# Optimization experiments

Hardware: AMD Instinct MI355X
Metric: run time of the kernel (lower is better)

Reference implementation:

```python
import jax, jax.numpy as jnp
import numpy as np

B, S, D, H = 4, 2048, 1024, 16
DH = D // H  # 64


def setup_inputs() -> dict:
    key = jax.random.key(0)
    ks = jax.random.split(key, 8)
    sc = 1.0 / np.sqrt(D)
    return {
        "hidden_states": jax.random.normal(ks[0], (B, S, D), jnp.float32),
        "attention_mask": jnp.zeros((B, 1, 1, S), jnp.float32),
        "Wq": jax.random.normal(ks[1], (D, D), jnp.float32) * sc,
        "bq": jnp.zeros((D,), jnp.float32),
        "Wk": jax.random.normal(ks[2], (D, D), jnp.float32) * sc,
        "bk": jnp.zeros((D,), jnp.float32),
        "Wv": jax.random.normal(ks[3], (D, D), jnp.float32) * sc,
        "bv": jnp.zeros((D,), jnp.float32),
    }


def _heads(x):
    # [B,S,D] -> [B,H,S,DH]
    b, s, _ = x.shape
    return x.reshape(b, s, H, DH).transpose(0, 2, 1, 3)


def reference(hidden_states, attention_mask, Wq, bq, Wk, bk, Wv, bv):
    q = _heads(hidden_states @ Wq + bq)
    k = _heads(hidden_states @ Wk + bk)
    v = _heads(hidden_states @ Wv + bv)
    scores = jnp.einsum('bhqd,bhkd->bhqk', q, k) / jnp.sqrt(jnp.float32(DH))
    scores = scores + attention_mask  # additive mask, broadcast
    probs = jax.nn.softmax(scores, axis=-1)  # dropout is identity in eval
    out = jnp.einsum('bhqk,bhkd->bhqd', probs, v)
    b, h, s, dh = out.shape
    return out.transpose(0, 2, 1, 3).reshape(b, s, h * dh)
```

## Files before the change

### kernel.cpp

```cpp
#include <hip/hip_runtime.h>
#include <hip/hip_bf16.h>
#include <cstdint>

typedef _Float16 f16;
typedef f16 f16x8 __attribute__((ext_vector_type(8)));
typedef f16 f16x4 __attribute__((ext_vector_type(4)));
typedef float f32x4 __attribute__((ext_vector_type(4)));

#define MFMA16(a, b, c) __builtin_amdgcn_mfma_f32_16x16x32_f16((a), (b), (c), 0, 0, 0)

constexpr int Bc = 4, Sc = 2048, Dc = 1024, Hc = 16, DHc = 64;

typedef __attribute__((address_space(1))) const uint32_t gbl_u32;
typedef __attribute__((address_space(3))) uint32_t lds_u32;
__device__ __forceinline__ void gld_lds16(const void* g, void* l) {
  __builtin_amdgcn_global_load_lds((gbl_u32*)g, (lds_u32*)l, 16, 0, 0);
}

__global__ __launch_bounds__(256) void cast_w_kernel(
    const float* __restrict__ Wq, const float* __restrict__ Wk,
    const float* __restrict__ Wv, f16* __restrict__ Wt) {
  __shared__ __align__(16) f16 T[64][66];
  const int z = blockIdx.z;
  const float* W = (z == 0) ? Wq : (z == 1) ? Wk : Wv;
  const int n0 = blockIdx.x * 64, k0 = blockIdx.y * 64;
  const int t = threadIdx.x;
#pragma unroll
  for (int p = 0; p < 4; p++) {
    int idx = t + p * 256;
    int r = idx >> 4, c = idx & 15;
    float4 v = *(const float4*)(W + (size_t)(k0 + r) * Dc + n0 + c * 4);
    T[r][c * 4 + 0] = (f16)v.x;
    T[r][c * 4 + 1] = (f16)v.y;
    T[r][c * 4 + 2] = (f16)v.z;
    T[r][c * 4 + 3] = (f16)v.w;
  }
  __syncthreads();
#pragma unroll
  for (int p = 0; p < 2; p++) {
    int idx = t + p * 256;
    int n = idx >> 3, c = idx & 7;
    f16x8 tmp;
#pragma unroll
    for (int j = 0; j < 8; j++) tmp[j] = T[c * 8 + j][n];
    *(f16x8*)(Wt + ((size_t)z * Dc + n0 + n) * Dc + k0 + c * 8) = tmp;
  }
}

__global__ __launch_bounds__(256) void cast_x_kernel(const float* __restrict__ X,
                                                     f16* __restrict__ X16) {
  size_t i = ((size_t)blockIdx.x * 256 + threadIdx.x) * 8;
  float4 a = *(const float4*)(X + i);
  float4 b = *(const float4*)(X + i + 4);
  f16x8 h;
  h[0] = (f16)a.x; h[1] = (f16)a.y; h[2] = (f16)a.z; h[3] = (f16)a.w;
  h[4] = (f16)b.x; h[5] = (f16)b.y; h[6] = (f16)b.z; h[7] = (f16)b.w;
  *(f16x8*)(X16 + i) = h;
}

__global__ __launch_bounds__(256) void qkv_gemm_kernel(
    const f16* __restrict__ X16, const f16* __restrict__ Wt,
    const float* __restrict__ bq, const float* __restrict__ bk,
    const float* __restrict__ bv, f16* __restrict__ Qo, f16* __restrict__ Ko,
    f16* __restrict__ Vo) {
  const int z = blockIdx.z;
  const f16* W = Wt + (size_t)z * Dc * Dc;
  const float* bias = (z == 0) ? bq : (z == 1) ? bk : bv;

  const int n0 = blockIdx.x * 128, m0 = blockIdx.y * 128;
  __shared__ __align__(16) f16 Xs[128 * 32];
  __shared__ __align__(16) f16 Ws[128 * 32];

  const int t = threadIdx.x;
  const int wave = t >> 6, lane = t & 63;
  const int l16 = lane & 15, quad = lane >> 4;
  const int wm = (wave >> 1) * 64, wn = (wave & 1) * 64;

  f32x4 acc[4][4];
#pragma unroll
  for (int i = 0; i < 4; i++)
#pragma unroll
    for (int j = 0; j < 4; j++) acc[i][j] = (f32x4){0.f, 0.f, 0.f, 0.f};

  for (int k0 = 0; k0 < Dc; k0 += 32) {
#pragma unroll
    for (int p = 0; p < 2; p++) {
      int cb = p * 256 + wave * 64;
      int chunk = cb + lane;
      int row = chunk >> 2, c8 = (chunk & 3) * 8;
      gld_lds16(X16 + (size_t)(m0 + row) * Dc + k0 + c8, (f16*)Xs + (size_t)cb * 8);
      gld_lds16(W + (size_t)(n0 + row) * Dc + k0 + c8, (f16*)Ws + (size_t)cb * 8);
    }
    __syncthreads();

    f16x8 aF[4], bF[4];
#pragma unroll
    for (int mt = 0; mt < 4; mt++)
      aF[mt] = *(const f16x8*)(&Xs[(wm + mt * 16 + l16) * 32 + quad * 8]);
#pragma unroll
    for (int nt = 0; nt < 4; nt++)
      bF[nt] = *(const f16x8*)(&Ws[(wn + nt * 16 + l16) * 32 + quad * 8]);
#pragma unroll
    for (int mt = 0; mt < 4; mt++)
#pragma unroll
      for (int nt = 0; nt < 4; nt++)
        acc[mt][nt] = MFMA16(aF[mt], bF[nt], acc[mt][nt]);
    __syncthreads();
  }

#pragma unroll
  for (int nt = 0; nt < 4; nt++) {
    int col = n0 + wn + nt * 16 + l16;
    float bval = bias[col];
    int h = col >> 6, d = col & 63;
    if (z == 2) {
#pragma unroll
      for (int mt = 0; mt < 4; mt++) {
        int m = m0 + wm + mt * 16 + quad * 4;
        int b = m >> 11, sbase = m & 2047;
        f16x4 pk;
#pragma unroll
        for (int r = 0; r < 4; r++) pk[r] = (f16)(acc[mt][nt][r] + bval);
        *(f16x4*)(Vo + (((size_t)(b * Hc + h)) * DHc + d) * Sc + sbase) = pk;
      }
    } else {
      const float sc = (z == 0) ? 0.125f : 1.0f;
      f16* O = (z == 0) ? Qo : Ko;
#pragma unroll
      for (int mt = 0; mt < 4; mt++) {
#pragma unroll
        for (int r = 0; r < 4; r++) {
          int m = m0 + wm + mt * 16 + quad * 4 + r;
          int b = m >> 11, s = m & 2047;
          O[(((size_t)(b * Hc + h)) * Sc + s) * DHc + d] =
              (f16)((acc[mt][nt][r] + bval) * sc);
        }
      }
    }
  }
}

__global__ __launch_bounds__(256) void flash_kernel(
    const f16* __restrict__ Q, const f16* __restrict__ K,
    const f16* __restrict__ Vt, const float* __restrict__ mask,
    float* __restrict__ out) {
  const int bh = blockIdx.y;
  const int b = bh >> 4, h = bh & 15;
  const int t = threadIdx.x;
  const int wave = t >> 6, lane = t & 63;
  const int l16 = lane & 15, quad = lane >> 4;
  const int qbase = blockIdx.x * 128 + wave * 32;

  __shared__ __align__(16) f16 Ks[2][4096];
  __shared__ __align__(16) f16 Vs[2][4096];
  __shared__ __align__(16) float Ms[2048];
  __shared__ __align__(16) f16 Pbuf[4][16][76];

  const f16* Kb = K + (size_t)bh * Sc * DHc;
  const f16* Vb = Vt + (size_t)bh * DHc * Sc;
  const float* mrow = mask + (size_t)b * Sc;

  const int qsw8 = (quad ^ ((l16 >> 1) & 3)) * 8;

  auto stageKV = [&](int c0, int buf) {
#pragma unroll
    for (int p = 0; p < 2; p++) {
      int cb = p * 256 + wave * 64;
      int i = cb + lane;
      int half = i >> 8, row = (i >> 2) & 63, q8 = i & 3;
      int q8g = q8 ^ ((row >> 1) & 3);
      gld_lds16(Kb + (size_t)(c0 + row) * DHc + half * 32 + q8g * 8,
                &Ks[buf][cb * 8]);
      gld_lds16(Vb + (size_t)row * Sc + c0 + half * 32 + q8g * 8,
                &Vs[buf][cb * 8]);
    }
  };

  f16x8 qa[2][2];
#pragma unroll
  for (int mt = 0; mt < 2; mt++) {
    const f16* qb = Q + ((size_t)bh * Sc + qbase + mt * 16 + l16) * DHc;
    qa[mt][0] = *(const f16x8*)(qb + quad * 8);
    qa[mt][1] = *(const f16x8*)(qb + 32 + quad * 8);
  }

  stageKV(0, 0);
#pragma unroll
  for (int p = 0; p < 2; p++) {
    int cb = p * 256 + wave * 64;
    gld_lds16(mrow + (size_t)(cb + lane) * 4, &Ms[cb * 4]);
  }
  __syncthreads();

  float l_acc[2] = {0.f, 0.f};
  f32x4 o[2][4];
#pragma unroll
  for (int mt = 0; mt < 2; mt++)
#pragma unroll
    for (int dt = 0; dt < 4; dt++) o[mt][dt] = (f32x4){0.f, 0.f, 0.f, 0.f};

  for (int c = 0; c < 32; c++) {
    const int buf = c & 1;
    if (c < 31) stageKV((c + 1) * 64, buf ^ 1);

    f16x8 ka[4][2];
#pragma unroll
    for (int nt = 0; nt < 4; nt++) {
      int rb = (nt * 16 + l16) * 32 + qsw8;
      ka[nt][0] = *(const f16x8*)(&Ks[buf][rb]);
      ka[nt][1] = *(const f16x8*)(&Ks[buf][2048 + rb]);
    }
    float4 mv[4];
#pragma unroll
    for (int nt = 0; nt < 4; nt++)
      mv[nt] = *(const float4*)(&Ms[c * 64 + nt * 16 + quad * 4]);

    f32x4 s0[4];
#pragma unroll
    for (int nt = 0; nt < 4; nt++) {
      f32x4 a = (f32x4){mv[nt].x, mv[nt].y, mv[nt].z, mv[nt].w};
      a = MFMA16(ka[nt][0], qa[0][0], a);
      a = MFMA16(ka[nt][1], qa[0][1], a);
      s0[nt] = a;
    }
    {
      float ls = 0.f;
#pragma unroll
      for (int nt = 0; nt < 4; nt++) {
        f16x4 pk;
#pragma unroll
        for (int r = 0; r < 4; r++) {
          float p = __expf(s0[nt][r]);
          ls += p;
          pk[r] = (f16)p;
        }
        *(f16x4*)(&Pbuf[wave][l16][nt * 16 + quad * 4]) = pk;
      }
      l_acc[0] += ls;
    }

    f32x4 s1[4];
#pragma unroll
    for (int nt = 0; nt < 4; nt++) {
      f32x4 a = (f32x4){mv[nt].x, mv[nt].y, mv[nt].z, mv[nt].w};
      a = MFMA16(ka[nt][0], qa[1][0], a);
      a = MFMA16(ka[nt][1], qa[1][1], a);
      s1[nt] = a;
    }

    f16x8 pa0, pa1;
    {
      const f16* prow = &Pbuf[wave][l16][0];
      f16x4 a0 = *(const f16x4*)(prow + quad * 8);
      f16x4 a1 = *(const f16x4*)(prow + quad * 8 + 4);
      f16x4 b0 = *(const f16x4*)(prow + 32 + quad * 8);
      f16x4 b1 = *(const f16x4*)(prow + 32 + quad * 8 + 4);
      pa0 = __builtin_shufflevector(a0, a1, 0, 1, 2, 3, 4, 5, 6, 7);
      pa1 = __builtin_shufflevector(b0, b1, 0, 1, 2, 3, 4, 5, 6, 7);
    }
    f16x8 vb[4][2];
#pragma unroll
    for (int dt = 0; dt < 4; dt++) {
      int rb = (dt * 16 + l16) * 32 + qsw8;
      vb[dt][0] = *(const f16x8*)(&Vs[buf][rb]);
      vb[dt][1] = *(const f16x8*)(&Vs[buf][2048 + rb]);
    }
#pragma unroll
    for (int dt = 0; dt < 4; dt++) {
      o[0][dt] = MFMA16(pa0, vb[dt][0], o[0][dt]);
      o[0][dt] = MFMA16(pa1, vb[dt][1], o[0][dt]);
    }

    {
      float ls = 0.f;
#pragma unroll
      for (int nt = 0; nt < 4; nt++) {
        f16x4 pk;
#pragma unroll
        for (int r = 0; r < 4; r++) {
          float p = __expf(s1[nt][r]);
          ls += p;
          pk[r] = (f16)p;
        }
        *(f16x4*)(&Pbuf[wave][l16][nt * 16 + quad * 4]) = pk;
      }
      l_acc[1] += ls;
    }
    {
      const f16* prow = &Pbuf[wave][l16][0];
      f16x4 a0 = *(const f16x4*)(prow + quad * 8);
      f16x4 a1 = *(const f16x4*)(prow + quad * 8 + 4);
      f16x4 b0 = *(const f16x4*)(prow + 32 + quad * 8);
      f16x4 b1 = *(const f16x4*)(prow + 32 + quad * 8 + 4);
      f16x8 qa0p = __builtin_shufflevector(a0, a1, 0, 1, 2, 3, 4, 5, 6, 7);
      f16x8 qa1p = __builtin_shufflevector(b0, b1, 0, 1, 2, 3, 4, 5, 6, 7);
#pragma unroll
      for (int dt = 0; dt < 4; dt++) {
        o[1][dt] = MFMA16(qa0p, vb[dt][0], o[1][dt]);
        o[1][dt] = MFMA16(qa1p, vb[dt][1], o[1][dt]);
      }
    }

    __syncthreads();
  }

#pragma unroll
  for (int mt = 0; mt < 2; mt++) {
    l_acc[mt] += __shfl_xor(l_acc[mt], 16);
    l_acc[mt] += __shfl_xor(l_acc[mt], 32);
  }
#pragma unroll
  for (int mt = 0; mt < 2; mt++) {
    float inv[4];
#pragma unroll
    for (int r = 0; r < 4; r++)
      inv[r] = 1.0f / __shfl(l_acc[mt], quad * 4 + r);
#pragma unroll
    for (int dt = 0; dt < 4; dt++) {
      int col = h * 64 + dt * 16 + l16;
#pragma unroll
      for (int r = 0; r < 4; r++) {
        int row = qbase + mt * 16 + quad * 4 + r;
        out[((size_t)b * Sc + row) * Dc + col] = o[mt][dt][r] * inv[r];
      }
    }
  }
}

extern "C" void kernel_launch(void* const* d_in, const int* in_sizes, int n_in,
                              void* d_out, int out_size, void* d_ws,
                              size_t ws_size, hipStream_t stream) {
  (void)in_sizes; (void)n_in; (void)out_size; (void)ws_size;
  const float* hidden = (const float*)d_in[0];
  const float* mask   = (const float*)d_in[1];
  const float* Wq     = (const float*)d_in[2];
  const float* bq     = (const float*)d_in[3];
  const float* Wk     = (const float*)d_in[4];
  const float* bk     = (const float*)d_in[5];
  const float* Wv     = (const float*)d_in[6];
  const float* bv     = (const float*)d_in[7];
  float* out = (float*)d_out;

  uint8_t* w = (uint8_t*)d_ws;
  f16* Wt   = (f16*)(w);
  f16* X16  = (f16*)(w + (size_t)6 * 1024 * 1024);
  f16* Q16  = (f16*)(w + (size_t)22 * 1024 * 1024);
  f16* K16  = (f16*)(w + (size_t)38 * 1024 * 1024);
  f16* Vt16 = (f16*)(w + (size_t)54 * 1024 * 1024);

  cast_w_kernel<<<dim3(16, 16, 3), 256, 0, stream>>>(Wq, Wk, Wv, Wt);
  cast_x_kernel<<<4096, 256, 0, stream>>>(hidden, X16);
  qkv_gemm_kernel<<<dim3(8, 64, 3), 256, 0, stream>>>(X16, Wt, bq, bk, bv,
                                                      Q16, K16, Vt16);
  flash_kernel<<<dim3(16, 64), 256, 0, stream>>>(Q16, K16, Vt16, mask, out);
}
```

Baseline: 287.2 us.

## Keep P in registers via 16x16x16 MFMA, drop LDS P round-trip and mask staging

```diff
diff --git a/kernel.cpp b/kernel.cpp
--- a/kernel.cpp
+++ b/kernel.cpp
@@ -8,6 +8,7 @@
 typedef float f32x4 __attribute__((ext_vector_type(4)));
 
 #define MFMA16(a, b, c) __builtin_amdgcn_mfma_f32_16x16x32_f16((a), (b), (c), 0, 0, 0)
+#define MFMA16K16(a, b, c) __builtin_amdgcn_mfma_f32_16x16x16f16((a), (b), (c), 0, 0, 0)
 
 constexpr int Bc = 4, Sc = 2048, Dc = 1024, Hc = 16, DHc = 64;
 
@@ -153,14 +154,13 @@
 
   __shared__ __align__(16) f16 Ks[2][4096];
   __shared__ __align__(16) f16 Vs[2][4096];
-  __shared__ __align__(16) float Ms[2048];
-  __shared__ __align__(16) f16 Pbuf[4][16][76];
 
   const f16* Kb = K + (size_t)bh * Sc * DHc;
   const f16* Vb = Vt + (size_t)bh * DHc * Sc;
   const float* mrow = mask + (size_t)b * Sc;
 
   const int qsw8 = (quad ^ ((l16 >> 1) & 3)) * 8;
+  const int vsw = (l16 >> 1) & 3;
 
   auto stageKV = [&](int c0, int buf) {
 #pragma unroll
@@ -185,11 +185,6 @@
   }
 
   stageKV(0, 0);
-#pragma unroll
-  for (int p = 0; p < 2; p++) {
-    int cb = p * 256 + wave * 64;
-    gld_lds16(mrow + (size_t)(cb + lane) * 4, &Ms[cb * 4]);
-  }
   __syncthreads();
 
   float l_acc[2] = {0.f, 0.f};
@@ -201,6 +196,10 @@
 
   for (int c = 0; c < 32; c++) {
     const int buf = c & 1;
+    float4 mv[4];
+#pragma unroll
+    for (int nt = 0; nt < 4; nt++)
+      mv[nt] = *(const float4*)(mrow + c * 64 + nt * 16 + quad * 4);
     if (c < 31) stageKV((c + 1) * 64, buf ^ 1);
 
     f16x8 ka[4][2];
@@ -210,94 +209,46 @@
       ka[nt][0] = *(const f16x8*)(&Ks[buf][rb]);
       ka[nt][1] = *(const f16x8*)(&Ks[buf][2048 + rb]);
     }
-    float4 mv[4];
-#pragma unroll
-    for (int nt = 0; nt < 4; nt++)
-      mv[nt] = *(const float4*)(&Ms[c * 64 + nt * 16 + quad * 4]);
-
-    f32x4 s0[4];
+
+    f32x4 s0[4], s1[4];
 #pragma unroll
     for (int nt = 0; nt < 4; nt++) {
       f32x4 a = (f32x4){mv[nt].x, mv[nt].y, mv[nt].z, mv[nt].w};
       a = MFMA16(ka[nt][0], qa[0][0], a);
       a = MFMA16(ka[nt][1], qa[0][1], a);
       s0[nt] = a;
-    }
-    {
-      float ls = 0.f;
+      f32x4 a2 = (f32x4){mv[nt].x, mv[nt].y, mv[nt].z, mv[nt].w};
+      a2 = MFMA16(ka[nt][0], qa[1][0], a2);
+      a2 = MFMA16(ka[nt][1], qa[1][1], a2);
+      s1[nt] = a2;
+    }
+
+    f16x4 pA[2][4];
+#pragma unroll
+    for (int nt = 0; nt < 4; nt++) {
+      float ls0 = 0.f, ls1 = 0.f;
+      f16x4 p0, p1;
+#pragma unroll
+      for (int r = 0; r < 4; r++) {
+        float e0 = __expf(s0[nt][r]);
+        float e1 = __expf(s1[nt][r]);
+        ls0 += e0; ls1 += e1;
+        p0[r] = (f16)e0; p1[r] = (f16)e1;
+      }
+      pA[0][nt] = p0; pA[1][nt] = p1;
+      l_acc[0] += ls0; l_acc[1] += ls1;
+    }
+
+#pragma unroll
+    for (int dt = 0; dt < 4; dt++) {
+      int dh = dt * 16 + l16;
 #pragma unroll
       for (int nt = 0; nt < 4; nt++) {
-        f16x4 pk;
-#pragma unroll
-        for (int r = 0; r < 4; r++) {
-          float p = __expf(s0[nt][r]);
-          ls += p;
-          pk[r] = (f16)p;
-        }
-        *(f16x4*)(&Pbuf[wave][l16][nt * 16 + quad * 4]) = pk;
-      }
-      l_acc[0] += ls;
-    }
-
-    f32x4 s1[4];
-#pragma unroll
-    for (int nt = 0; nt < 4; nt++) {
-      f32x4 a = (f32x4){mv[nt].x, mv[nt].y, mv[nt].z, mv[nt].w};
-      a = MFMA16(ka[nt][0], qa[1][0], a);
-      a = MFMA16(ka[nt][1], qa[1][1], a);
-      s1[nt] = a;
-    }
-
-    f16x8 pa0, pa1;
-    {
-      const f16* prow = &Pbuf[wave][l16][0];
-      f16x4 a0 = *(const f16x4*)(prow + quad * 8);
-      f16x4 a1 = *(const f16x4*)(prow + quad * 8 + 4);
-      f16x4 b0 = *(const f16x4*)(prow + 32 + quad * 8);
-      f16x4 b1 = *(const f16x4*)(prow + 32 + quad * 8 + 4);
-      pa0 = __builtin_shufflevector(a0, a1, 0, 1, 2, 3, 4, 5, 6, 7);
-      pa1 = __builtin_shufflevector(b0, b1, 0, 1, 2, 3, 4, 5, 6, 7);
-    }
-    f16x8 vb[4][2];
-#pragma unroll
-    for (int dt = 0; dt < 4; dt++) {
-      int rb = (dt * 16 + l16) * 32 + qsw8;
-      vb[dt][0] = *(const f16x8*)(&Vs[buf][rb]);
-      vb[dt][1] = *(const f16x8*)(&Vs[buf][2048 + rb]);
-    }
-#pragma unroll
-    for (int dt = 0; dt < 4; dt++) {
-      o[0][dt] = MFMA16(pa0, vb[dt][0], o[0][dt]);
-      o[0][dt] = MFMA16(pa1, vb[dt][1], o[0][dt]);
-    }
-
-    {
-      float ls = 0.f;
-#pragma unroll
-      for (int nt = 0; nt < 4; nt++) {
-        f16x4 pk;
-#pragma unroll
-        for (int r = 0; r < 4; r++) {
-          float p = __expf(s1[nt][r]);
-          ls += p;
-          pk[r] = (f16)p;
-        }
-        *(f16x4*)(&Pbuf[wave][l16][nt * 16 + quad * 4]) = pk;
-      }
-      l_acc[1] += ls;
-    }
-    {
-      const f16* prow = &Pbuf[wave][l16][0];
-      f16x4 a0 = *(const f16x4*)(prow + quad * 8);
-      f16x4 a1 = *(const f16x4*)(prow + quad * 8 + 4);
-      f16x4 b0 = *(const f16x4*)(prow + 32 + quad * 8);
-      f16x4 b1 = *(const f16x4*)(prow + 32 + quad * 8 + 4);
-      f16x8 qa0p = __builtin_shufflevector(a0, a1, 0, 1, 2, 3, 4, 5, 6, 7);
-      f16x8 qa1p = __builtin_shufflevector(b0, b1, 0, 1, 2, 3, 4, 5, 6, 7);
-#pragma unroll
-      for (int dt = 0; dt < 4; dt++) {
-        o[1][dt] = MFMA16(qa0p, vb[dt][0], o[1][dt]);
-        o[1][dt] = MFMA16(qa1p, vb[dt][1], o[1][dt]);
+        int q8g = (((nt & 1) * 2 + (quad >> 1)) ^ vsw) * 8;
+        f16x4 vB = *(const f16x4*)(
+            &Vs[buf][(nt >> 1) * 2048 + dh * 32 + q8g + (quad & 1) * 4]);
+        o[0][dt] = MFMA16K16(pA[0][nt], vB, o[0][dt]);
+        o[1][dt] = MFMA16K16(pA[1][nt], vB, o[1][dt]);
       }
     }
 
```

Result: no change. 286.2 us (-0.3%).
